# Optimization experiments

Measured on AMD Instinct MI355X. Metric: run time of the kernel, lower is better.

The kernel has to match this reference:

```python
import jax, jax.numpy as jnp
import numpy as np

MV = 16  # multivector dim of Cl(3,0,1), basis blades indexed by bitmask over (e0,e1,e2,e3)

def _pc(x):
    return bin(x).count("1")

def _sign(a, b):
    # canonical reordering sign for concatenating blade a then blade b
    s = 0
    a >>= 1
    while a:
        s += _pc(a & b)
        a >>= 1
    return -1.0 if (s & 1) else 1.0

def _tables():
    GP = np.zeros((MV, MV, MV), np.float32)  # geometric product structure constants
    OP = np.zeros((MV, MV, MV), np.float32)  # outer (wedge) product
    for a in range(MV):
        for b in range(MV):
            if not (a & b & 1):  # e0^2 = 0 (degenerate metric), e1..e3 square to +1
                GP[a, b, a ^ b] = _sign(a, b)
            if (a & b) == 0:
                OP[a, b, a | b] = _sign(a, b)
    # right complement dual: blade a -> comp c with a ^ c = pseudoscalar, sign so a ^ comp(a) = +e0123
    D = np.zeros((MV, MV), np.float32)
    for a in range(MV):
        c = a ^ (MV - 1)
        D[c, a] = _sign(a, c)
    # join(a,b) = undual(dual(a) ^ dual(b)); D is a signed permutation so D^{-1} = D^T
    J = np.einsum("pi,qj,pqr,kr->ijk", D, D, OP, D.T)
    # equivariant linear basis: 5 grade projections + 4 left-e0-multiplication maps (per grade 0..3)
    mats = []
    for g in range(5):
        M = np.zeros((MV, MV), np.float32)
        for a in range(MV):
            if _pc(a) == g:
                M[a, a] = 1.0
        mats.append(M)
    for g in range(4):
        M = np.array(GP[1], np.float32)  # GP[1][x,y]: coeff at e_y of e0 * e_x
        for a in range(MV):
            if _pc(a) != g:
                M[a, :] = 0.0
        mats.append(M)
    return jnp.asarray(np.stack(mats)), jnp.asarray(GP), jnp.asarray(J)

BLADE, GP_T, JOIN_T = _tables()  # BLADE: [9,16,16]

def _equi_linear(w, x):
    # w: [out_ch, in_ch, 9], x: [..., in_ch, 16] -> [..., out_ch, 16]
    return jnp.einsum("jib,bxy,...ix->...jy", w, BLADE, x)

def setup_inputs() -> dict:
    key = jax.random.key(0)
    ks = jax.random.split(key, 6)
    B, N, C_IN, C_HID = 8, 2048, 64, 128
    x = jax.random.normal(ks[0], (B, N, C_IN, MV), jnp.float32)
    ref = jax.random.normal(ks[1], (B, N, 1, MV), jnp.float32)
    wshape = (C_HID // 2, C_IN, BLADE.shape[0])
    return {
        "x": x,
        "ref": ref,
        "w_g1": jax.random.uniform(ks[2], wshape, jnp.float32),
        "w_g2": jax.random.uniform(ks[3], wshape, jnp.float32),
        "w_j1": jax.random.uniform(ks[4], wshape, jnp.float32),
        "w_j2": jax.random.uniform(ks[5], wshape, jnp.float32),
    }

def reference(x, ref, w_g1, w_g2, w_j1, w_j2):
    g1 = _equi_linear(w_g1, x)
    g2 = _equi_linear(w_g2, x)
    gp = jnp.einsum("...ci,ijk,...cj->...ck", g1, GP_T, g2) * 1e-5
    j1 = _equi_linear(w_j1, x)
    j2 = _equi_linear(w_j2, x)
    # equivariant join, scaled by pseudoscalar (e0123) component of the reference multivector
    jn = ref[..., 15:16] * jnp.einsum("...ci,ijk,...cj->...ck", j1, JOIN_T, j2)
    return jnp.concatenate([gp, jn], axis=-2)  # [B, N, hidden_mv_channels, 16]
```

## Files before the change

kernel.cpp:

```cpp
#include <hip/hip_runtime.h>

typedef unsigned short u16;
typedef unsigned int   u32;
typedef __attribute__((ext_vector_type(4))) float f32x4;
typedef __attribute__((ext_vector_type(8))) short bf16x8;

constexpr int pcf(int x){ int c=0; while(x){ c += x&1; x>>=1; } return c; }
constexpr int signexp(int a,int b){ int s=0; a>>=1; while(a){ s += pcf(a&b); a>>=1; } return s&1; }
constexpr float sgnf(int a,int b){ return signexp(a,b) ? -1.0f : 1.0f; }
constexpr float sDf(int a){ return sgnf(a, a^15); }

struct Tbl {
  float gp[16][16];
  float jn[16][16];
};
constexpr Tbl make_tbl(){
  Tbl t{};
  for(int a=0;a<16;a++){
    for(int b=0;b<16;b++){
      t.gp[a][b] = (a & b & 1) ? 0.0f : sgnf(a,b);
      t.jn[a][b] = ((a|b)==15) ? sDf(a)*sDf(b)*sDf(a&b)*sgnf(a^15,b^15) : 0.0f;
    }
  }
  return t;
}
constexpr Tbl TBL = make_tbl();
constexpr int PC[16] = {0,1,1,2,1,2,2,3,1,2,2,3,2,3,3,4};

__device__ __forceinline__ u16 f2bf(float f){
  union { float f; unsigned u; } v; v.f = f;
  unsigned r = v.u + 0x7fffu + ((v.u >> 16) & 1u);
  return (u16)(r >> 16);
}

__global__ __launch_bounds__(256) void k_wb(const float* __restrict__ wg1,
                                            const float* __restrict__ wg2,
                                            const float* __restrict__ wj1,
                                            const float* __restrict__ wj2,
                                            u16* __restrict__ wb)
{
  const int e = blockIdx.x*256 + threadIdx.x;
  const int t   = e / 36864;
  const int rem = e % 36864;
  const int c = rem / 576, r2 = rem % 576, i = r2 / 9, b = r2 % 9;
  const float* wp = (t < 2) ? (t ? wg2 : wg1) : ((t == 2) ? wj1 : wj2);
  const float v = wp[rem];
  const int dst = ((t*9 + b)*8 + (c>>4)*2 + (i>>5))*512
                + (16*((i>>3)&3) + (c&15))*8 + (i&7);
  wb[dst] = f2bf(v);
}

__global__ __launch_bounds__(512) void k_fused(const float* __restrict__ x,
                                               const u16* __restrict__ wb,
                                               const float* __restrict__ ref,
                                               float* __restrict__ out)
{
  __shared__ __align__(16) u16 lds[16384];

  const int t = threadIdx.x, w = t >> 6, l = t & 63;
  const int pair = w >> 2, nt = w & 3;
  const int t1 = pair*2, t2 = t1 + 1;
  const int tile = blockIdx.x;

  {
    const int pp = t & 15;
    const int ip = t >> 4;
    const int d32 = (ip >> 4)*256 + (16*((ip >> 2) & 3) + pp)*4 + (ip & 3);

    float4 X0[8];
    const float4* s4 = (const float4*)(x + ((size_t)(tile*16 + pp))*1024 + ip*32);
    #pragma unroll
    for (int k = 0; k < 8; ++k) X0[k] = s4[k];

    u32* lw = (u32*)lds;
    const float* v = (const float*)X0;
    #pragma unroll
    for (int y = 0; y < 16; ++y)
      lw[y*512 + d32] = (u32)f2bf(v[y]) | ((u32)f2bf(v[16 + y]) << 16);
  }

  __syncthreads();

  f32x4 acc1[16], acc2[16];
  #pragma unroll
  for (int y = 0; y < 16; ++y) {
    acc1[y] = (f32x4){0.f,0.f,0.f,0.f};
    acc2[y] = (f32x4){0.f,0.f,0.f,0.f};
  }

  #pragma unroll
  for (int y = 0; y < 16; ++y) {
    #pragma unroll
    for (int kt = 0; kt < 2; ++kt) {
      bf16x8 a  = *(const bf16x8*)&lds[y*1024 + kt*512 + l*8];
      bf16x8 b1 = *(const bf16x8*)(wb + ((size_t)((t1*9 + PC[y])*8 + nt*2 + kt))*512 + l*8);
      bf16x8 b2 = *(const bf16x8*)(wb + ((size_t)((t2*9 + PC[y])*8 + nt*2 + kt))*512 + l*8);
      acc1[y] = __builtin_amdgcn_mfma_f32_16x16x32_bf16(a, b1, acc1[y], 0, 0, 0);
      acc2[y] = __builtin_amdgcn_mfma_f32_16x16x32_bf16(a, b2, acc2[y], 0, 0, 0);
    }
    if (y & 1) {
      const int bb = 4 + PC[y];
      #pragma unroll
      for (int kt = 0; kt < 2; ++kt) {
        bf16x8 a  = *(const bf16x8*)&lds[(y^1)*1024 + kt*512 + l*8];
        bf16x8 b1 = *(const bf16x8*)(wb + ((size_t)((t1*9 + bb)*8 + nt*2 + kt))*512 + l*8);
        bf16x8 b2 = *(const bf16x8*)(wb + ((size_t)((t2*9 + bb)*8 + nt*2 + kt))*512 + l*8);
        acc1[y] = __builtin_amdgcn_mfma_f32_16x16x32_bf16(a, b1, acc1[y], 0, 0, 0);
        acc2[y] = __builtin_amdgcn_mfma_f32_16x16x32_bf16(a, b2, acc2[y], 0, 0, 0);
      }
    }
  }

  __syncthreads();

  f32x4* scr = (f32x4*)lds;
  const int pg = l >> 4, c16 = l & 15;

  #pragma unroll
  for (int r = 0; r < 4; ++r) {
    float g1[16], g2[16];
    #pragma unroll
    for (int y = 0; y < 16; ++y) { g1[y] = acc1[y][r]; g2[y] = acc2[y][r]; }
    float o[16];
    #pragma unroll
    for (int k = 0; k < 16; ++k) o[k] = 0.0f;

    if (pair == 0) {
      #pragma unroll
      for (int a = 0; a < 16; ++a)
        #pragma unroll
        for (int b = 0; b < 16; ++b) {
          const float sg = TBL.gp[a][b];
          if (sg != 0.0f) o[a ^ b] += sg * g1[a] * g2[b];
        }
      #pragma unroll
      for (int k = 0; k < 16; ++k) o[k] *= 1e-5f;
    } else {
      const float r15 = ref[(size_t)(tile*16 + pg*4 + r)*16 + 15];
      #pragma unroll
      for (int a = 0; a < 16; ++a)
        #pragma unroll
        for (int b = 0; b < 16; ++b) {
          const float sg = TBL.jn[a][b];
          if (sg != 0.0f) o[a & b] += sg * g1[a] * g2[b];
        }
      #pragma unroll
      for (int k = 0; k < 16; ++k) o[k] *= r15;
    }

    #pragma unroll
    for (int j = 0; j < 4; ++j) {
      const int loc = pg*64 + c16*4 + j;
      const int f4s = loc ^ ((loc >> 3) & 7);
      scr[w*256 + f4s] = (f32x4){o[j*4], o[j*4+1], o[j*4+2], o[j*4+3]};
    }

    #pragma unroll
    for (int q = 0; q < 4; ++q) {
      const int loc = q*64 + l;
      const int f4s = loc ^ ((loc >> 3) & 7);
      const f32x4 v = scr[w*256 + f4s];
      float4* dst = (float4*)(out + ((size_t)(tile*16 + q*4 + r)*128 + pair*64 + nt*16)*16) + l;
      *dst = make_float4(v[0], v[1], v[2], v[3]);
    }
  }
}

#define P_TILE 8
#define I_CHUNK 4

__global__ __launch_bounds__(256) void gbl_fused(
    const float* __restrict__ x, const float* __restrict__ ref,
    const float* __restrict__ wg1, const float* __restrict__ wg2,
    const float* __restrict__ wj1, const float* __restrict__ wj2,
    float* __restrict__ out)
{
  __shared__ float lds_x[P_TILE * 1024];
  __shared__ float lds_w[2 * I_CHUNK * 576];

  const int t    = threadIdx.x;
  const int tile = blockIdx.x >> 1;
  const int tau  = blockIdx.x & 1;
  const float* __restrict__ w1g = tau ? wj1 : wg1;
  const float* __restrict__ w2g = tau ? wj2 : wg2;

  const int c  = t & 63;
  const int ps = t >> 6;

  {
    const float4* __restrict__ gx = (const float4*)(x + (size_t)tile * (P_TILE * 1024));
    float4* lx = (float4*)lds_x;
    #pragma unroll
    for (int k = 0; k < 8; ++k) lx[t + k * 256] = gx[t + k * 256];
  }

  float acc1[2][16], acc2[2][16];
  #pragma unroll
  for (int s = 0; s < 2; ++s)
    #pragma unroll
    for (int y = 0; y < 16; ++y) { acc1[s][y] = 0.0f; acc2[s][y] = 0.0f; }

  for (int i0 = 0; i0 < 64; i0 += I_CHUNK) {
    __syncthreads();
    #pragma unroll
    for (int k = 0; k < 9; ++k) {
      const int e  = t + k * 256;
      const int cc = e / 36;
      const int r  = e % 36;
      const int il = r / 9;
      const int b  = r % 9;
      lds_w[ il            * 576 + cc * 9 + b] = w1g[cc * 576 + i0 * 9 + r];
      lds_w[(I_CHUNK + il) * 576 + cc * 9 + b] = w2g[cc * 576 + i0 * 9 + r];
    }
    __syncthreads();

    #pragma unroll
    for (int il = 0; il < I_CHUNK; ++il) {
      float w1[9], w2[9];
      #pragma unroll
      for (int b = 0; b < 9; ++b) {
        w1[b] = lds_w[ il            * 576 + c * 9 + b];
        w2[b] = lds_w[(I_CHUNK + il) * 576 + c * 9 + b];
      }
      #pragma unroll
      for (int s = 0; s < 2; ++s) {
        const int p = ps + s * 4;
        const float4* xr = (const float4*)&lds_x[p * 1024 + (i0 + il) * 16];
        const float4 xa = xr[0], xb = xr[1], xc4 = xr[2], xd = xr[3];
        const float xv[16] = { xa.x, xa.y, xa.z, xa.w, xb.x, xb.y, xb.z, xb.w,
                               xc4.x, xc4.y, xc4.z, xc4.w, xd.x, xd.y, xd.z, xd.w };
        #pragma unroll
        for (int y = 0; y < 16; ++y) {
          acc1[s][y] += w1[PC[y]] * xv[y];
          acc2[s][y] += w2[PC[y]] * xv[y];
        }
        #pragma unroll
        for (int y = 1; y < 16; y += 2) {
          acc1[s][y] += w1[4 + PC[y]] * xv[y ^ 1];
          acc2[s][y] += w2[4 + PC[y]] * xv[y ^ 1];
        }
      }
    }
  }

  #pragma unroll
  for (int s = 0; s < 2; ++s) {
    const int p = ps + s * 4;
    const size_t pos = (size_t)tile * P_TILE + p;
    float o[16];
    #pragma unroll
    for (int k = 0; k < 16; ++k) o[k] = 0.0f;

    if (tau == 0) {
      #pragma unroll
      for (int a = 0; a < 16; ++a)
        #pragma unroll
        for (int b = 0; b < 16; ++b) {
          const float sg = TBL.gp[a][b];
          if (sg != 0.0f) o[a ^ b] += sg * acc1[s][a] * acc2[s][b];
        }
      #pragma unroll
      for (int k = 0; k < 16; ++k) o[k] *= 1e-5f;
    } else {
      const float r15 = ref[pos * 16 + 15];
      #pragma unroll
      for (int a = 0; a < 16; ++a)
        #pragma unroll
        for (int b = 0; b < 16; ++b) {
          const float sg = TBL.jn[a][b];
          if (sg != 0.0f) o[a & b] += sg * acc1[s][a] * acc2[s][b];
        }
      #pragma unroll
      for (int k = 0; k < 16; ++k) o[k] *= r15;
    }

    float4* po = (float4*)(out + (pos * 128 + (size_t)tau * 64 + c) * 16);
    po[0] = make_float4(o[0],  o[1],  o[2],  o[3]);
    po[1] = make_float4(o[4],  o[5],  o[6],  o[7]);
    po[2] = make_float4(o[8],  o[9],  o[10], o[11]);
    po[3] = make_float4(o[12], o[13], o[14], o[15]);
  }
}

extern "C" void kernel_launch(void* const* d_in, const int* in_sizes, int n_in,
                              void* d_out, int out_size, void* d_ws, size_t ws_size,
                              hipStream_t stream) {
  const float* x   = (const float*)d_in[0];
  const float* ref = (const float*)d_in[1];
  const float* wg1 = (const float*)d_in[2];
  const float* wg2 = (const float*)d_in[3];
  const float* wj1 = (const float*)d_in[4];
  const float* wj2 = (const float*)d_in[5];
  float* outp = (float*)d_out;

  const int npos = in_sizes[0] / (64 * 16);

  if (ws_size >= 294912 && (npos % 16) == 0) {
    u16* wb = (u16*)d_ws;
    k_wb   <<<576, 256, 0, stream>>>(wg1, wg2, wj1, wj2, wb);
    k_fused<<<npos / 16, 512, 0, stream>>>(x, wb, ref, outp);
  } else {
    const int grid = (npos / P_TILE) * 2;
    gbl_fused<<<grid, 256, 0, stream>>>(x, ref, wg1, wg2, wj1, wj2, outp);
  }
}
```

Measured before the change: 68.80 us.

## Make fused kernel persistent with register-prefetched next tile and grade-grouped weights

Replaces the one-tile-per-block kernel with a persistent kernel of 256 blocks, each looping over several 16-position tiles. The next tile's x is loaded into registers while the current tile is computed, and converted to bf16 LDS only after the epilogue. Weight fragments are loaded once per grade group and reused across all blades of that grade instead of being reloaded per blade. Waves per EU is pinned at 2, and explicit barriers with sched_barrier are added. The cost is extra register pressure from holding the prefetched tile, plus fewer blocks available to hide latency.

```diff
diff --git a/kernel.cpp b/kernel.cpp
--- a/kernel.cpp
+++ b/kernel.cpp
@@ -27,11 +27,21 @@
 constexpr Tbl TBL = make_tbl();
 constexpr int PC[16] = {0,1,1,2,1,2,2,3,1,2,2,3,2,3,3,4};
 
+constexpr int GRADE_Y[5][6] = {{0,0,0,0,0,0},{1,2,4,8,0,0},{3,5,6,9,10,12},{7,11,13,14,0,0},{15,0,0,0,0,0}};
+constexpr int GRADE_N[5] = {1,4,6,4,1};
+
 __device__ __forceinline__ u16 f2bf(float f){
   union { float f; unsigned u; } v; v.f = f;
   unsigned r = v.u + 0x7fffu + ((v.u >> 16) & 1u);
   return (u16)(r >> 16);
 }
+
+#define BARRIER() do {                                          \
+  asm volatile("s_waitcnt lgkmcnt(0)" ::: "memory");            \
+  __builtin_amdgcn_sched_barrier(0);                            \
+  __builtin_amdgcn_s_barrier();                                 \
+  __builtin_amdgcn_sched_barrier(0);                            \
+} while (0)
 
 __global__ __launch_bounds__(256) void k_wb(const float* __restrict__ wg1,
                                             const float* __restrict__ wg2,
@@ -50,118 +60,145 @@
   wb[dst] = f2bf(v);
 }
 
-__global__ __launch_bounds__(512) void k_fused(const float* __restrict__ x,
-                                               const u16* __restrict__ wb,
-                                               const float* __restrict__ ref,
-                                               float* __restrict__ out)
+__global__ __launch_bounds__(512)
+__attribute__((amdgpu_waves_per_eu(2, 2)))
+void k_pipe(const float* __restrict__ x, const u16* __restrict__ wb,
+            const float* __restrict__ ref, float* __restrict__ out,
+            int tpb)
 {
-  __shared__ __align__(16) u16 lds[16384];
+  __shared__ __align__(16) u16 F[16384];
 
   const int t = threadIdx.x, w = t >> 6, l = t & 63;
   const int pair = w >> 2, nt = w & 3;
   const int t1 = pair*2, t2 = t1 + 1;
-  const int tile = blockIdx.x;
-
-  {
-    const int pp = t & 15;
-    const int ip = t >> 4;
-    const int d32 = (ip >> 4)*256 + (16*((ip >> 2) & 3) + pp)*4 + (ip & 3);
-
-    float4 X0[8];
+  const int tile0 = blockIdx.x * tpb;
+
+  const int pp = t & 15;
+  const int ip = t >> 4;
+  const int d32 = (ip >> 4)*256 + (16*((ip >> 2) & 3) + pp)*4 + (ip & 3);
+
+  float4 X[8];
+
+  auto loadX = [&](int tile) {
     const float4* s4 = (const float4*)(x + ((size_t)(tile*16 + pp))*1024 + ip*32);
     #pragma unroll
-    for (int k = 0; k < 8; ++k) X0[k] = s4[k];
-
-    u32* lw = (u32*)lds;
-    const float* v = (const float*)X0;
+    for (int k = 0; k < 8; ++k) X[k] = s4[k];
+  };
+  auto convert = [&]() {
+    u32* lw = (u32*)F;
+    const float* v = (const float*)X;
     #pragma unroll
     for (int y = 0; y < 16; ++y)
       lw[y*512 + d32] = (u32)f2bf(v[y]) | ((u32)f2bf(v[16 + y]) << 16);
-  }
-
-  __syncthreads();
-
-  f32x4 acc1[16], acc2[16];
-  #pragma unroll
-  for (int y = 0; y < 16; ++y) {
-    acc1[y] = (f32x4){0.f,0.f,0.f,0.f};
-    acc2[y] = (f32x4){0.f,0.f,0.f,0.f};
-  }
-
-  #pragma unroll
-  for (int y = 0; y < 16; ++y) {
-    #pragma unroll
-    for (int kt = 0; kt < 2; ++kt) {
-      bf16x8 a  = *(const bf16x8*)&lds[y*1024 + kt*512 + l*8];
-      bf16x8 b1 = *(const bf16x8*)(wb + ((size_t)((t1*9 + PC[y])*8 + nt*2 + kt))*512 + l*8);
-      bf16x8 b2 = *(const bf16x8*)(wb + ((size_t)((t2*9 + PC[y])*8 + nt*2 + kt))*512 + l*8);
-      acc1[y] = __builtin_amdgcn_mfma_f32_16x16x32_bf16(a, b1, acc1[y], 0, 0, 0);
-      acc2[y] = __builtin_amdgcn_mfma_f32_16x16x32_bf16(a, b2, acc2[y], 0, 0, 0);
-    }
-    if (y & 1) {
-      const int bb = 4 + PC[y];
+  };
+
+  loadX(tile0);
+  convert();
+  if (tpb > 1) loadX(tile0 + 1);
+  BARRIER();
+
+  for (int s = 0; s < tpb; ++s) {
+    f32x4 acc1[16], acc2[16];
+    #pragma unroll
+    for (int y = 0; y < 16; ++y) {
+      acc1[y] = (f32x4){0.f,0.f,0.f,0.f};
+      acc2[y] = (f32x4){0.f,0.f,0.f,0.f};
+    }
+
+    #pragma unroll
+    for (int g = 0; g < 5; ++g) {
+      bf16x8 bg1[2], bg2[2], be1[2], be2[2];
       #pragma unroll
       for (int kt = 0; kt < 2; ++kt) {
-        bf16x8 a  = *(const bf16x8*)&lds[(y^1)*1024 + kt*512 + l*8];
-        bf16x8 b1 = *(const bf16x8*)(wb + ((size_t)((t1*9 + bb)*8 + nt*2 + kt))*512 + l*8);
-        bf16x8 b2 = *(const bf16x8*)(wb + ((size_t)((t2*9 + bb)*8 + nt*2 + kt))*512 + l*8);
-        acc1[y] = __builtin_amdgcn_mfma_f32_16x16x32_bf16(a, b1, acc1[y], 0, 0, 0);
-        acc2[y] = __builtin_amdgcn_mfma_f32_16x16x32_bf16(a, b2, acc2[y], 0, 0, 0);
-      }
-    }
-  }
-
-  __syncthreads();
-
-  f32x4* scr = (f32x4*)lds;
-  const int pg = l >> 4, c16 = l & 15;
-
-  #pragma unroll
-  for (int r = 0; r < 4; ++r) {
-    float g1[16], g2[16];
-    #pragma unroll
-    for (int y = 0; y < 16; ++y) { g1[y] = acc1[y][r]; g2[y] = acc2[y][r]; }
-    float o[16];
-    #pragma unroll
-    for (int k = 0; k < 16; ++k) o[k] = 0.0f;
-
-    if (pair == 0) {
-      #pragma unroll
-      for (int a = 0; a < 16; ++a)
-        #pragma unroll
-        for (int b = 0; b < 16; ++b) {
-          const float sg = TBL.gp[a][b];
-          if (sg != 0.0f) o[a ^ b] += sg * g1[a] * g2[b];
-        }
-      #pragma unroll
-      for (int k = 0; k < 16; ++k) o[k] *= 1e-5f;
-    } else {
-      const float r15 = ref[(size_t)(tile*16 + pg*4 + r)*16 + 15];
-      #pragma unroll
-      for (int a = 0; a < 16; ++a)
-        #pragma unroll
-        for (int b = 0; b < 16; ++b) {
-          const float sg = TBL.jn[a][b];
-          if (sg != 0.0f) o[a & b] += sg * g1[a] * g2[b];
-        }
-      #pragma unroll
-      for (int k = 0; k < 16; ++k) o[k] *= r15;
-    }
-
-    #pragma unroll
-    for (int j = 0; j < 4; ++j) {
-      const int loc = pg*64 + c16*4 + j;
-      const int f4s = loc ^ ((loc >> 3) & 7);
-      scr[w*256 + f4s] = (f32x4){o[j*4], o[j*4+1], o[j*4+2], o[j*4+3]};
-    }
-
-    #pragma unroll
-    for (int q = 0; q < 4; ++q) {
-      const int loc = q*64 + l;
-      const int f4s = loc ^ ((loc >> 3) & 7);
-      const f32x4 v = scr[w*256 + f4s];
-      float4* dst = (float4*)(out + ((size_t)(tile*16 + q*4 + r)*128 + pair*64 + nt*16)*16) + l;
-      *dst = make_float4(v[0], v[1], v[2], v[3]);
+        bg1[kt] = *(const bf16x8*)(wb + ((size_t)((t1*9 + g)*8 + nt*2 + kt))*512 + l*8);
+        bg2[kt] = *(const bf16x8*)(wb + ((size_t)((t2*9 + g)*8 + nt*2 + kt))*512 + l*8);
+      }
+      if (g >= 1) {
+        #pragma unroll
+        for (int kt = 0; kt < 2; ++kt) {
+          be1[kt] = *(const bf16x8*)(wb + ((size_t)((t1*9 + 4+g)*8 + nt*2 + kt))*512 + l*8);
+          be2[kt] = *(const bf16x8*)(wb + ((size_t)((t2*9 + 4+g)*8 + nt*2 + kt))*512 + l*8);
+        }
+      }
+      #pragma unroll
+      for (int yi = 0; yi < GRADE_N[g]; ++yi) {
+        const int y = GRADE_Y[g][yi];
+        #pragma unroll
+        for (int kt = 0; kt < 2; ++kt) {
+          bf16x8 a = *(const bf16x8*)&F[y*1024 + kt*512 + l*8];
+          acc1[y] = __builtin_amdgcn_mfma_f32_16x16x32_bf16(a, bg1[kt], acc1[y], 0, 0, 0);
+          acc2[y] = __builtin_amdgcn_mfma_f32_16x16x32_bf16(a, bg2[kt], acc2[y], 0, 0, 0);
+        }
+        if (y & 1) {
+          #pragma unroll
+          for (int kt = 0; kt < 2; ++kt) {
+            bf16x8 a = *(const bf16x8*)&F[(y^1)*1024 + kt*512 + l*8];
+            acc1[y] = __builtin_amdgcn_mfma_f32_16x16x32_bf16(a, be1[kt], acc1[y], 0, 0, 0);
+            acc2[y] = __builtin_amdgcn_mfma_f32_16x16x32_bf16(a, be2[kt], acc2[y], 0, 0, 0);
+          }
+        }
+      }
+    }
+
+    BARRIER();
+
+    const int tile = tile0 + s;
+    f32x4* scr = (f32x4*)F;
+    const int pg = l >> 4, c16 = l & 15;
+
+    #pragma unroll
+    for (int r = 0; r < 4; ++r) {
+      float g1[16], g2[16];
+      #pragma unroll
+      for (int y = 0; y < 16; ++y) { g1[y] = acc1[y][r]; g2[y] = acc2[y][r]; }
+      float o[16];
+      #pragma unroll
+      for (int k = 0; k < 16; ++k) o[k] = 0.0f;
+
+      if (pair == 0) {
+        #pragma unroll
+        for (int a = 0; a < 16; ++a)
+          #pragma unroll
+          for (int b = 0; b < 16; ++b) {
+            const float sg = TBL.gp[a][b];
+            if (sg != 0.0f) o[a ^ b] += sg * g1[a] * g2[b];
+          }
+        #pragma unroll
+        for (int k = 0; k < 16; ++k) o[k] *= 1e-5f;
+      } else {
+        const float r15 = ref[(size_t)(tile*16 + pg*4 + r)*16 + 15];
+        #pragma unroll
+        for (int a = 0; a < 16; ++a)
+          #pragma unroll
+          for (int b = 0; b < 16; ++b) {
+            const float sg = TBL.jn[a][b];
+            if (sg != 0.0f) o[a & b] += sg * g1[a] * g2[b];
+          }
+        #pragma unroll
+        for (int k = 0; k < 16; ++k) o[k] *= r15;
+      }
+
+      #pragma unroll
+      for (int j = 0; j < 4; ++j) {
+        const int loc = pg*64 + c16*4 + j;
+        const int f4s = loc ^ ((loc >> 3) & 7);
+        scr[w*256 + f4s] = (f32x4){o[j*4], o[j*4+1], o[j*4+2], o[j*4+3]};
+      }
+      #pragma unroll
+      for (int q = 0; q < 4; ++q) {
+        const int loc = q*64 + l;
+        const int f4s = loc ^ ((loc >> 3) & 7);
+        const f32x4 v = scr[w*256 + f4s];
+        float4* dst = (float4*)(out + ((size_t)(tile*16 + q*4 + r)*128 + pair*64 + nt*16)*16) + l;
+        *dst = make_float4(v[0], v[1], v[2], v[3]);
+      }
+    }
+
+    if (s + 1 < tpb) {
+      BARRIER();
+      convert();
+      if (s + 2 < tpb) loadX(tile0 + s + 2);
+      BARRIER();
     }
   }
 }
@@ -296,9 +333,13 @@
   const int npos = in_sizes[0] / (64 * 16);
 
   if (ws_size >= 294912 && (npos % 16) == 0) {
+    const int tiles = npos / 16;
+    int grid, tpb;
+    if      (tiles % 256 == 0) { grid = 256;   tpb = tiles / 256; }
+    else                       { grid = tiles; tpb = 1; }
     u16* wb = (u16*)d_ws;
-    k_wb   <<<576, 256, 0, stream>>>(wg1, wg2, wj1, wj2, wb);
-    k_fused<<<npos / 16, 512, 0, stream>>>(x, wb, ref, outp);
+    k_wb  <<<576, 256, 0, stream>>>(wg1, wg2, wj1, wj2, wb);
+    k_pipe<<<grid, 512, 0, stream>>>(x, wb, ref, outp, tpb);
   } else {
     const int grid = (npos / P_TILE) * 2;
     gbl_fused<<<grid, 256, 0, stream>>>(x, ref, wg1, wg2, wj1, wj2, outp);
```

Result: slower. 133.8 us (+94.5%).
